# Kernel optimization log

Hardware: AMD Instinct MI355X
Metric: run time of the kernel (lower is better)

## Reference

```python
import jax, jax.numpy as jnp
import numpy as np

N = 100000   # nodes
E = 300000   # directed edges
IN_DIM = 10
HID = 384
OUT_DIM = 3
T = 5
BN_EPS = 1e-5


def setup_inputs() -> dict:
    key = jax.random.key(0)
    ks = jax.random.split(key, 32)
    i = iter(range(32))
    nxt = lambda: ks[next(i)]
    d = {}
    d["x"] = jax.random.normal(nxt(), (N, IN_DIM), dtype=jnp.float32)
    d["edge_index"] = jax.random.randint(nxt(), (2, E), 0, N, dtype=jnp.int32)
    s = 0.05
    # SAGEConv layer 0 (in_dim -> hid); lin_l has bias, lin_r has no bias (PyG defaults)
    d["W_l0"] = jax.random.normal(nxt(), (HID, IN_DIM), dtype=jnp.float32) * s
    d["b_l0"] = jnp.zeros((HID,), dtype=jnp.float32)
    d["W_r0"] = jax.random.normal(nxt(), (HID, IN_DIM), dtype=jnp.float32) * s
    # SAGEConv layers 1..T-1 (hid -> hid), stacked
    d["W_l"] = jax.random.normal(nxt(), (T - 1, HID, HID), dtype=jnp.float32) * s
    d["b_l"] = jnp.zeros((T - 1, HID), dtype=jnp.float32)
    d["W_r"] = jax.random.normal(nxt(), (T - 1, HID, HID), dtype=jnp.float32) * s
    # per-layer BatchNorm (eval mode: running stats)
    d["bn_g"] = jnp.ones((T, HID), dtype=jnp.float32)
    d["bn_b"] = jnp.zeros((T, HID), dtype=jnp.float32)
    d["bn_m"] = jax.random.normal(nxt(), (T, HID), dtype=jnp.float32) * 0.1
    d["bn_v"] = jax.random.uniform(nxt(), (T, HID), dtype=jnp.float32, minval=0.5, maxval=1.5)
    # projection MLP: Linear->BN->ReLU->Linear->BN->ReLU->Linear
    d["Wp0"] = jax.random.normal(nxt(), (HID, HID), dtype=jnp.float32) * s
    d["bp0"] = jnp.zeros((HID,), dtype=jnp.float32)
    d["Wp1"] = jax.random.normal(nxt(), (HID, HID), dtype=jnp.float32) * s
    d["bp1"] = jnp.zeros((HID,), dtype=jnp.float32)
    d["Wp2"] = jax.random.normal(nxt(), (OUT_DIM, HID), dtype=jnp.float32) * s
    d["bp2"] = jnp.zeros((OUT_DIM,), dtype=jnp.float32)
    d["pbn_g"] = jnp.ones((2, HID), dtype=jnp.float32)
    d["pbn_b"] = jnp.zeros((2, HID), dtype=jnp.float32)
    d["pbn_m"] = jax.random.normal(nxt(), (2, HID), dtype=jnp.float32) * 0.1
    d["pbn_v"] = jax.random.uniform(nxt(), (2, HID), dtype=jnp.float32, minval=0.5, maxval=1.5)
    return d


def _bn(x, g, b, m, v):
    return (x - m) * jax.lax.rsqrt(v + BN_EPS) * g + b


def _sage(x, src, dst, Wl, bl, Wr):
    # mean aggregation of neighbor features, then lin_l(agg) + lin_r(x), L2-normalized
    msg = jax.ops.segment_sum(x[src], dst, num_segments=N)            # [N, F]
    cnt = jax.ops.segment_sum(jnp.ones_like(dst, dtype=x.dtype), dst, num_segments=N)
    agg = msg / jnp.maximum(cnt, 1.0)[:, None]
    out = agg @ Wl.T + bl + x @ Wr.T
    nrm = jnp.linalg.norm(out, axis=-1, keepdims=True)
    return out / jnp.maximum(nrm, 1e-12)


def reference(x, edge_index, W_l0, b_l0, W_r0, W_l, b_l, W_r,
              bn_g, bn_b, bn_m, bn_v,
              Wp0, bp0, Wp1, bp1, Wp2, bp2,
              pbn_g, pbn_b, pbn_m, pbn_v):
    src, dst = edge_index[0], edge_index[1]
    h = x
    for t in range(T):  # T=5, fixed small loop over structurally distinct layers
        if t == 0:
            h = _sage(h, src, dst, W_l0, b_l0, W_r0)
        else:
            h = _sage(h, src, dst, W_l[t - 1], b_l[t - 1], W_r[t - 1])
        h = jax.nn.elu(_bn(h, bn_g[t], bn_b[t], bn_m[t], bn_v[t]))
        # dropout is identity in eval mode
    # projection MLP
    h = jax.nn.relu(_bn(h @ Wp0.T + bp0, pbn_g[0], pbn_b[0], pbn_m[0], pbn_v[0]))
    h = jax.nn.relu(_bn(h @ Wp1.T + bp1, pbn_g[1], pbn_b[1], pbn_m[1], pbn_v[1]))
    return h @ Wp2.T + bp2  # [N, 3]
```

## Files before the change

kernel.cpp:

```cpp
#include <hip/hip_runtime.h>
#include <hip/hip_bf16.h>

#define N_NODES 100000
#define N_EDGES 300000
#define IN_DIM 10
#define HID 384
#define OUT_DIM 3
#define T_LAYERS 5
#define BN_EPS 1e-5f

typedef __attribute__((ext_vector_type(8))) short short8;
typedef __attribute__((ext_vector_type(4))) float floatx4;

__device__ __forceinline__ float bf16f(short v) {
  return __uint_as_float(((unsigned)(unsigned short)v) << 16);
}

__device__ __forceinline__ void gld_lds16(const void* g, void* l) {
  __builtin_amdgcn_global_load_lds(
      (const __attribute__((address_space(1))) void*)g,
      (__attribute__((address_space(3))) void*)l, 16, 0, 0);
}


__global__ void count_k(const int* __restrict__ dst, int* __restrict__ cnt, int E) {
  int e = blockIdx.x * blockDim.x + threadIdx.x;
  if (e < E) atomicAdd(&cnt[dst[e]], 1);
}

__global__ void scan_partial_k(const int* __restrict__ cnt, int* __restrict__ bsum, int n) {
  int t = threadIdx.x;
  int i = blockIdx.x * 1024 + t;
  int v = (i < n) ? cnt[i] : 0;
  #pragma unroll
  for (int off = 1; off < 64; off <<= 1) v += __shfl_xor(v, off);
  __shared__ int ws[16];
  if ((t & 63) == 0) ws[t >> 6] = v;
  __syncthreads();
  if (t == 0) {
    int s = 0;
    #pragma unroll
    for (int w = 0; w < 16; ++w) s += ws[w];
    bsum[blockIdx.x] = s;
  }
}

__global__ void scan_small_k(int* __restrict__ bsum, int P) {
  __shared__ int s[1024];
  int t = threadIdx.x;
  int v = (t < P) ? bsum[t] : 0;
  s[t] = v;
  __syncthreads();
  for (int off = 1; off < 1024; off <<= 1) {
    int add = (t >= off) ? s[t - off] : 0;
    __syncthreads();
    s[t] += add;
    __syncthreads();
  }
  if (t < P) bsum[t] = s[t] - v;
}

__global__ void scan_final_k(const int* __restrict__ cnt, const int* __restrict__ bsum,
                             int* __restrict__ row_off, int n) {
  int t = threadIdx.x, lane = t & 63, wv = t >> 6;
  int i = blockIdx.x * 1024 + t;
  int v = (i < n) ? cnt[i] : 0;
  int x = v;
  #pragma unroll
  for (int off = 1; off < 64; off <<= 1) {
    int y = __shfl_up(x, off);
    if (lane >= off) x += y;
  }
  __shared__ int ws[16];
  if (lane == 63) ws[wv] = x;
  __syncthreads();
  if (t == 0) {
    int a = 0;
    #pragma unroll
    for (int w = 0; w < 16; ++w) { int tmp = ws[w]; ws[w] = a; a += tmp; }
  }
  __syncthreads();
  int excl = (x - v) + ws[wv] + bsum[blockIdx.x];
  if (i <= n) row_off[i] = excl;
}

__global__ void fill_k(const int* __restrict__ src, const int* __restrict__ dst,
                       const int* __restrict__ row_off, int* __restrict__ cursor,
                       int* __restrict__ csr, int E) {
  int e = blockIdx.x * blockDim.x + threadIdx.x;
  if (e < E) {
    int d = dst[e];
    int pos = atomicAdd(&cursor[d], 1);
    csr[row_off[d] + pos] = src[e];
  }
}


__global__ void conv_k(const float* __restrict__ src, __hip_bfloat16* __restrict__ dst, int n) {
  int i = blockIdx.x * blockDim.x + threadIdx.x;
  if (i < n) dst[i] = __float2bfloat16(src[i]);
}

__global__ void pack0_k(const float* __restrict__ x, const float* __restrict__ agg10,
                        __hip_bfloat16* __restrict__ X2, int n) {
  int i = blockIdx.x * blockDim.x + threadIdx.x;
  if (i < n * 64) {
    int node = i >> 6, k = i & 63;
    float v = (k < IN_DIM) ? x[node * IN_DIM + k]
              : (k < 2 * IN_DIM) ? agg10[node * IN_DIM + (k - IN_DIM)] : 0.f;
    X2[i] = __float2bfloat16(v);
  }
}

__global__ void packw0_k(const float* __restrict__ Wl, const float* __restrict__ Wr,
                         __hip_bfloat16* __restrict__ W2) {
  int i = blockIdx.x * blockDim.x + threadIdx.x;
  if (i < HID * 64) {
    int o = i >> 6, k = i & 63;
    float v = (k < IN_DIM) ? Wr[o * IN_DIM + k]
              : (k < 2 * IN_DIM) ? Wl[o * IN_DIM + (k - IN_DIM)]
              : 0.f;
    W2[i] = __float2bfloat16(v);
  }
}


__global__ void agg10_k(const float* __restrict__ x, const int* __restrict__ row_off,
                        const int* __restrict__ csr, float* __restrict__ agg10, int n) {
  int sub = threadIdx.x >> 5;
  int lane = threadIdx.x & 31;
  int node = blockIdx.x * 8 + sub;
  if (node >= n) return;
  int s = row_off[node], e = row_off[node + 1];
  if (lane < IN_DIM) {
    float acc = 0.f;
    for (int j = s; j < e; ++j) acc += x[csr[j] * IN_DIM + lane];
    float c = (float)max(e - s, 1);
    agg10[node * IN_DIM + lane] = acc / c;
  }
}

__global__ __launch_bounds__(256) void aggv_k(const __hip_bfloat16* __restrict__ h,
                                              const int* __restrict__ row_off,
                                              const int* __restrict__ csr,
                                              __hip_bfloat16* __restrict__ agg, int n) {
  int node = blockIdx.x * 4 + (threadIdx.x >> 6);
  if (node >= n) return;
  int lane = threadIdx.x & 63;
  if (lane >= 48) return;
  int s = row_off[node], e = row_off[node + 1];
  float acc[8] = {0.f, 0.f, 0.f, 0.f, 0.f, 0.f, 0.f, 0.f};
  for (int j = s; j < e; ++j) {
    const uint4 v = *(const uint4*)(h + (size_t)csr[j] * HID + lane * 8);
    uint u0 = v.x, u1 = v.y, u2 = v.z, u3 = v.w;
    acc[0] += __uint_as_float(u0 << 16);
    acc[1] += __uint_as_float(u0 & 0xffff0000u);
    acc[2] += __uint_as_float(u1 << 16);
    acc[3] += __uint_as_float(u1 & 0xffff0000u);
    acc[4] += __uint_as_float(u2 << 16);
    acc[5] += __uint_as_float(u2 & 0xffff0000u);
    acc[6] += __uint_as_float(u3 << 16);
    acc[7] += __uint_as_float(u3 & 0xffff0000u);
  }
  float invc = 1.f / (float)max(e - s, 1);
  uint out[4];
  #pragma unroll
  for (int q = 0; q < 4; ++q) {
    __hip_bfloat16 lo = __float2bfloat16(acc[2 * q] * invc);
    __hip_bfloat16 hi = __float2bfloat16(acc[2 * q + 1] * invc);
    out[q] = (uint)(*(unsigned short*)&lo) | ((uint)(*(unsigned short*)&hi) << 16);
  }
  *(uint4*)(agg + (size_t)node * HID + lane * 8) = make_uint4(out[0], out[1], out[2], out[3]);
}

template <int KTOT, bool DUAL, int EPI, bool FINAL>
__global__ __launch_bounds__(512, 4) void mfma_gemm_k(
    const __hip_bfloat16* __restrict__ A1, const __hip_bfloat16* __restrict__ B1,
    const __hip_bfloat16* __restrict__ A2, const __hip_bfloat16* __restrict__ B2,
    const float* __restrict__ bias,
    const float* __restrict__ bng, const float* __restrict__ bnb,
    const float* __restrict__ bnm, const float* __restrict__ bnv,
    __hip_bfloat16* __restrict__ out,
    const float* __restrict__ W3, const float* __restrict__ b3,
    float* __restrict__ out3) {
  __shared__ alignas(16) short smem[64 * 64 + HID * 64];
  short* sA = smem;
  short* sB = smem + 64 * 64;

  const int t = threadIdx.x;
  const int lane = t & 63;
  const int wv = t >> 6;
  const int n16 = lane & 15;
  const int quad = lane >> 4;
  const int row0 = blockIdx.x * 64;

  const int aRow = t >> 3;
  const int aG = (t & 7) ^ (aRow & 7);
  const int aOff = min(row0 + aRow, N_NODES - 1) * KTOT + aG * 8;
  int bOff[6];
  #pragma unroll
  for (int it = 0; it < 6; ++it) {
    int col = (wv * 6 + it) * 8 + (lane >> 3);
    int g = (lane & 7) ^ (col & 7);
    bOff[it] = col * KTOT + g * 8;
  }

  floatx4 acc[4][3];
  #pragma unroll
  for (int rt = 0; rt < 4; ++rt)
    #pragma unroll
    for (int ct = 0; ct < 3; ++ct) acc[rt][ct] = (floatx4)0.f;

  constexpr int KCH = KTOT / 64;
  constexpr int NCH = DUAL ? 2 * KCH : KCH;
  for (int c = 0; c < NCH; ++c) {
    const __hip_bfloat16* Ap;
    const __hip_bfloat16* Bp;
    int kc;
    if (!DUAL || c < KCH) { Ap = A1; Bp = B1; kc = c * 64; }
    else                  { Ap = A2; Bp = B2; kc = (c - KCH) * 64; }
    gld_lds16(Ap + aOff + kc, sA + wv * 512);
    #pragma unroll
    for (int it = 0; it < 6; ++it)
      gld_lds16(Bp + bOff[it] + kc, sB + (wv * 6 + it) * 512);
    __syncthreads();
    #pragma unroll
    for (int kh = 0; kh < 2; ++kh) {
      short8 af[4], bf[3];
      int g = kh * 4 + quad;
      #pragma unroll
      for (int rt = 0; rt < 4; ++rt) {
        int r = rt * 16 + n16;
        af[rt] = *(const short8*)&sA[r * 64 + ((g ^ (r & 7)) * 8)];
      }
      #pragma unroll
      for (int ct = 0; ct < 3; ++ct) {
        int cl = wv * 48 + ct * 16 + n16;
        bf[ct] = *(const short8*)&sB[cl * 64 + ((g ^ (cl & 7)) * 8)];
      }
      #pragma unroll
      for (int rt = 0; rt < 4; ++rt)
        #pragma unroll
        for (int ct = 0; ct < 3; ++ct)
          acc[rt][ct] = __builtin_amdgcn_mfma_f32_16x16x32_bf16(af[rt], bf[ct], acc[rt][ct], 0, 0, 0);
    }
    __syncthreads();
  }

  int gc[3];
  #pragma unroll
  for (int ct = 0; ct < 3; ++ct) {
    gc[ct] = wv * 48 + ct * 16 + n16;
    float bs = bias[gc[ct]];
    #pragma unroll
    for (int rt = 0; rt < 4; ++rt)
      #pragma unroll
      for (int rg = 0; rg < 4; ++rg) acc[rt][ct][rg] += bs;
  }

  if constexpr (EPI == 0) {
    float* red = (float*)smem;
    float inv[4][4];
    #pragma unroll
    for (int rt = 0; rt < 4; ++rt)
      #pragma unroll
      for (int rg = 0; rg < 4; ++rg) {
        float s = 0.f;
        #pragma unroll
        for (int ct = 0; ct < 3; ++ct) s += acc[rt][ct][rg] * acc[rt][ct][rg];
        #pragma unroll
        for (int off = 1; off < 16; off <<= 1) s += __shfl_xor(s, off);
        if (n16 == 0) red[wv * 64 + rt * 16 + quad * 4 + rg] = s;
      }
    __syncthreads();
    #pragma unroll
    for (int rt = 0; rt < 4; ++rt)
      #pragma unroll
      for (int rg = 0; rg < 4; ++rg) {
        int rl = rt * 16 + quad * 4 + rg;
        float ss = 0.f;
        #pragma unroll
        for (int w = 0; w < 8; ++w) ss += red[w * 64 + rl];
        inv[rt][rg] = 1.f / fmaxf(sqrtf(ss), 1e-12f);
      }
    #pragma unroll
    for (int rt = 0; rt < 4; ++rt)
      #pragma unroll
      for (int ct = 0; ct < 3; ++ct)
        #pragma unroll
        for (int rg = 0; rg < 4; ++rg) acc[rt][ct][rg] *= inv[rt][rg];
    __syncthreads();
  }

  constexpr int OS = 392;
  short* sO = smem;
  #pragma unroll
  for (int ct = 0; ct < 3; ++ct) {
    int col = gc[ct];
    float sc = bng[col] * rsqrtf(bnv[col] + BN_EPS);
    float sh = bnb[col] - bnm[col] * sc;
    #pragma unroll
    for (int rt = 0; rt < 4; ++rt)
      #pragma unroll
      for (int rg = 0; rg < 4; ++rg) {
        float xv = acc[rt][ct][rg] * sc + sh;
        if constexpr (EPI == 0)
          xv = xv > 0.f ? xv : expm1f(xv);
        else
          xv = fmaxf(xv, 0.f);
        __hip_bfloat16 bv = __float2bfloat16(xv);
        sO[(rt * 16 + quad * 4 + rg) * OS + col] = *(short*)&bv;
      }
  }
  __syncthreads();

  if constexpr (FINAL) {
    if (t < 192) {
      int row = t & 63, o = t >> 6;
      int grow = row0 + row;
      if (grow < N_NODES) {
        float s = 0.f;
        #pragma unroll
        for (int kb = 0; kb < 48; ++kb) {
          short8 hv = *(const short8*)&sO[row * OS + kb * 8];
          #pragma unroll
          for (int j = 0; j < 8; ++j) s += bf16f(hv[j]) * W3[o * HID + kb * 8 + j];
        }
        out3[grow * OUT_DIM + o] = s + b3[o];
      }
    }
  } else {
    #pragma unroll
    for (int it = 0; it < 6; ++it) {
      int e = t + it * 512;
      int row = e / 48, cs = e % 48;
      int grow = row0 + row;
      if (grow < N_NODES) {
        uint4 v = *(const uint4*)&sO[row * OS + cs * 8];
        *(uint4*)(out + (size_t)grow * HID + cs * 8) = v;
      }
    }
  }
}


extern "C" void kernel_launch(void* const* d_in, const int* in_sizes, int n_in,
                              void* d_out, int out_size, void* d_ws, size_t ws_size,
                              hipStream_t stream) {
  const float* x = (const float*)d_in[0];
  const int* ei = (const int*)d_in[1];
  const int* src = ei;
  const int* dst = ei + N_EDGES;
  const float* W_l0 = (const float*)d_in[2];
  const float* b_l0 = (const float*)d_in[3];
  const float* W_r0 = (const float*)d_in[4];
  const float* W_l = (const float*)d_in[5];
  const float* b_l = (const float*)d_in[6];
  const float* W_r = (const float*)d_in[7];
  const float* bn_g = (const float*)d_in[8];
  const float* bn_b = (const float*)d_in[9];
  const float* bn_m = (const float*)d_in[10];
  const float* bn_v = (const float*)d_in[11];
  const float* Wp0 = (const float*)d_in[12];
  const float* bp0 = (const float*)d_in[13];
  const float* Wp1 = (const float*)d_in[14];
  const float* bp1 = (const float*)d_in[15];
  const float* Wp2 = (const float*)d_in[16];
  const float* bp2 = (const float*)d_in[17];
  const float* pbn_g = (const float*)d_in[18];
  const float* pbn_b = (const float*)d_in[19];
  const float* pbn_m = (const float*)d_in[20];
  const float* pbn_v = (const float*)d_in[21];

  char* ws = (char*)d_ws;
  size_t off = 0;
  auto walloc = [&](size_t bytes) -> void* {
    void* p = ws + off;
    off = (off + bytes + 255) & ~(size_t)255;
    return p;
  };
  __hip_bfloat16* h   = (__hip_bfloat16*)walloc((size_t)N_NODES * HID * 2);
  __hip_bfloat16* agg = (__hip_bfloat16*)walloc((size_t)N_NODES * HID * 2);
  float* agg10 = (float*)agg;
  __hip_bfloat16* X2  = (__hip_bfloat16*)walloc((size_t)N_NODES * 64 * 2);
  __hip_bfloat16* W2  = (__hip_bfloat16*)walloc((size_t)HID * 64 * 2);
  __hip_bfloat16* WlB  = (__hip_bfloat16*)walloc((size_t)(T_LAYERS - 1) * HID * HID * 2);
  __hip_bfloat16* WrB  = (__hip_bfloat16*)walloc((size_t)(T_LAYERS - 1) * HID * HID * 2);
  __hip_bfloat16* Wp0B = (__hip_bfloat16*)walloc((size_t)HID * HID * 2);
  __hip_bfloat16* Wp1B = (__hip_bfloat16*)walloc((size_t)HID * HID * 2);
  int* cnt     = (int*)walloc((size_t)N_NODES * 4);
  int* row_off = (int*)walloc((size_t)(N_NODES + 1) * 4);
  int* cursor  = (int*)walloc((size_t)N_NODES * 4);
  int* csr     = (int*)walloc((size_t)N_EDGES * 4);
  int* bsum    = (int*)walloc(4096);

  hipMemsetAsync(cnt, 0, (size_t)N_NODES * 4, stream);
  hipMemsetAsync(cursor, 0, (size_t)N_NODES * 4, stream);

  const int NW = (T_LAYERS - 1) * HID * HID;
  conv_k<<<(NW + 255) / 256, 256, 0, stream>>>(W_l, WlB, NW);
  conv_k<<<(NW + 255) / 256, 256, 0, stream>>>(W_r, WrB, NW);
  conv_k<<<(HID * HID + 255) / 256, 256, 0, stream>>>(Wp0, Wp0B, HID * HID);
  conv_k<<<(HID * HID + 255) / 256, 256, 0, stream>>>(Wp1, Wp1B, HID * HID);
  packw0_k<<<(HID * 64 + 255) / 256, 256, 0, stream>>>(W_l0, W_r0, W2);

  count_k<<<(N_EDGES + 255) / 256, 256, 0, stream>>>(dst, cnt, N_EDGES);
  int P = (N_NODES + 1 + 1023) / 1024;
  scan_partial_k<<<P, 1024, 0, stream>>>(cnt, bsum, N_NODES);
  scan_small_k<<<1, 1024, 0, stream>>>(bsum, P);
  scan_final_k<<<P, 1024, 0, stream>>>(cnt, bsum, row_off, N_NODES);
  fill_k<<<(N_EDGES + 255) / 256, 256, 0, stream>>>(src, dst, row_off, cursor, csr, N_EDGES);

  const int GB = (N_NODES + 63) / 64;

  agg10_k<<<(N_NODES + 7) / 8, 256, 0, stream>>>(x, row_off, csr, agg10, N_NODES);
  pack0_k<<<(N_NODES * 64 + 255) / 256, 256, 0, stream>>>(x, agg10, X2, N_NODES);
  mfma_gemm_k<64, false, 0, false><<<GB, 512, 0, stream>>>(
      X2, W2, nullptr, nullptr, b_l0, bn_g, bn_b, bn_m, bn_v, h,
      nullptr, nullptr, nullptr);

  for (int t = 1; t < T_LAYERS; ++t) {
    aggv_k<<<(N_NODES + 3) / 4, 256, 0, stream>>>(h, row_off, csr, agg, N_NODES);
    mfma_gemm_k<HID, true, 0, false><<<GB, 512, 0, stream>>>(
        agg, WlB + (size_t)(t - 1) * HID * HID,
        h,   WrB + (size_t)(t - 1) * HID * HID,
        b_l + (size_t)(t - 1) * HID,
        bn_g + (size_t)t * HID, bn_b + (size_t)t * HID,
        bn_m + (size_t)t * HID, bn_v + (size_t)t * HID,
        h, nullptr, nullptr, nullptr);
  }

  mfma_gemm_k<HID, false, 1, false><<<GB, 512, 0, stream>>>(
      h, Wp0B, nullptr, nullptr, bp0, pbn_g, pbn_b, pbn_m, pbn_v, h,
      nullptr, nullptr, nullptr);
  mfma_gemm_k<HID, false, 1, true><<<GB, 512, 0, stream>>>(
      h, Wp1B, nullptr, nullptr, bp1, pbn_g + HID, pbn_b + HID, pbn_m + HID, pbn_v + HID, h,
      Wp2, bp2, (float*)d_out);
}
```

Baseline: 1.072 ms.

## Double-buffer A tile in MFMA GEMM with manual vmcnt waits and barriers

Adds a two-stage LDS buffer for the A tile, so the next chunk's A load is issued before the wait on the current chunk's loads. The __syncthreads pair is replaced by raw s_barrier with explicit s_waitcnt. The MFMA loop is restructured to load one B fragment at a time, and the inverse-norm array is scoped per row tile to cut register pressure. LDS is padded to 64KB, which may lower occupancy, and the hand-written vmcnt counting risks reading incomplete data if the compiler emits other loads.

```diff
diff --git a/kernel.cpp b/kernel.cpp
--- a/kernel.cpp
+++ b/kernel.cpp
@@ -183,9 +183,8 @@
     __hip_bfloat16* __restrict__ out,
     const float* __restrict__ W3, const float* __restrict__ b3,
     float* __restrict__ out3) {
-  __shared__ alignas(16) short smem[64 * 64 + HID * 64];
-  short* sA = smem;
-  short* sB = smem + 64 * 64;
+  __shared__ alignas(16) short smem[32768];
+  short* sB = smem + 8192;
 
   const int t = threadIdx.x;
   const int lane = t & 63;
@@ -213,38 +212,54 @@
 
   constexpr int KCH = KTOT / 64;
   constexpr int NCH = DUAL ? 2 * KCH : KCH;
+
+  gld_lds16(A1 + aOff, smem + wv * 512);
+
   for (int c = 0; c < NCH; ++c) {
-    const __hip_bfloat16* Ap;
     const __hip_bfloat16* Bp;
     int kc;
-    if (!DUAL || c < KCH) { Ap = A1; Bp = B1; kc = c * 64; }
-    else                  { Ap = A2; Bp = B2; kc = (c - KCH) * 64; }
-    gld_lds16(Ap + aOff + kc, sA + wv * 512);
+    if (!DUAL || c < KCH) { Bp = B1; kc = c * 64; }
+    else                  { Bp = B2; kc = (c - KCH) * 64; }
+
     #pragma unroll
     for (int it = 0; it < 6; ++it)
       gld_lds16(Bp + bOff[it] + kc, sB + (wv * 6 + it) * 512);
-    __syncthreads();
+
+    if (c + 1 < NCH) {
+      const __hip_bfloat16* Ap;
+      int kn;
+      int cn = c + 1;
+      if (!DUAL || cn < KCH) { Ap = A1; kn = cn * 64; }
+      else                   { Ap = A2; kn = (cn - KCH) * 64; }
+      gld_lds16(Ap + aOff + kn, smem + (cn & 1) * 4096 + wv * 512);
+      asm volatile("s_waitcnt vmcnt(1)" ::: "memory");
+    } else {
+      asm volatile("s_waitcnt vmcnt(0)" ::: "memory");
+    }
+    __builtin_amdgcn_sched_barrier(0);
+    __builtin_amdgcn_s_barrier();
+
+    const short* sAc = smem + (c & 1) * 4096;
     #pragma unroll
     for (int kh = 0; kh < 2; ++kh) {
-      short8 af[4], bf[3];
+      short8 af[4];
       int g = kh * 4 + quad;
       #pragma unroll
       for (int rt = 0; rt < 4; ++rt) {
         int r = rt * 16 + n16;
-        af[rt] = *(const short8*)&sA[r * 64 + ((g ^ (r & 7)) * 8)];
+        af[rt] = *(const short8*)&sAc[r * 64 + ((g ^ (r & 7)) * 8)];
       }
       #pragma unroll
       for (int ct = 0; ct < 3; ++ct) {
         int cl = wv * 48 + ct * 16 + n16;
-        bf[ct] = *(const short8*)&sB[cl * 64 + ((g ^ (cl & 7)) * 8)];
-      }
-      #pragma unroll
-      for (int rt = 0; rt < 4; ++rt)
-        #pragma unroll
-        for (int ct = 0; ct < 3; ++ct)
-          acc[rt][ct] = __builtin_amdgcn_mfma_f32_16x16x32_bf16(af[rt], bf[ct], acc[rt][ct], 0, 0, 0);
+        short8 bf = *(const short8*)&sB[cl * 64 + ((g ^ (cl & 7)) * 8)];
+        #pragma unroll
+        for (int rt = 0; rt < 4; ++rt)
+          acc[rt][ct] = __builtin_amdgcn_mfma_f32_16x16x32_bf16(af[rt], bf, acc[rt][ct], 0, 0, 0);
+      }
     }
-    __syncthreads();
+    __builtin_amdgcn_s_barrier();
+    asm volatile("" ::: "memory");
   }
 
   int gc[3];
@@ -260,7 +275,6 @@
 
   if constexpr (EPI == 0) {
     float* red = (float*)smem;
-    float inv[4][4];
     #pragma unroll
     for (int rt = 0; rt < 4; ++rt)
       #pragma unroll
@@ -274,21 +288,21 @@
       }
     __syncthreads();
     #pragma unroll
-    for (int rt = 0; rt < 4; ++rt)
+    for (int rt = 0; rt < 4; ++rt) {
+      float inv[4];
       #pragma unroll
       for (int rg = 0; rg < 4; ++rg) {
         int rl = rt * 16 + quad * 4 + rg;
         float ss = 0.f;
         #pragma unroll
         for (int w = 0; w < 8; ++w) ss += red[w * 64 + rl];
-        inv[rt][rg] = 1.f / fmaxf(sqrtf(ss), 1e-12f);
-      }
-    #pragma unroll
-    for (int rt = 0; rt < 4; ++rt)
+        inv[rg] = 1.f / fmaxf(sqrtf(ss), 1e-12f);
+      }
       #pragma unroll
       for (int ct = 0; ct < 3; ++ct)
         #pragma unroll
-        for (int rg = 0; rg < 4; ++rg) acc[rt][ct][rg] *= inv[rt][rg];
+        for (int rg = 0; rg < 4; ++rg) acc[rt][ct][rg] *= inv[rg];
+    }
     __syncthreads();
   }
 
```

After: 1.045 ms. 2.5% less time.
